# Optimization experiments

Hardware: AMD Instinct MI355X
Metric: run time of the kernel (lower is better)

## Reference

```python
import jax, jax.numpy as jnp
import numpy as np

B, N, DIM, HEADS = 8, 512, 512, 16
MAX_DIST, NG = 128, 32
RBF_STOP = 20.0
EPS = 1e-5


def _ln(x, g, b):
    m = jnp.mean(x, axis=-1, keepdims=True)
    v = jnp.mean((x - m) ** 2, axis=-1, keepdims=True)
    return (x - m) * jax.lax.rsqrt(v + EPS) * g + b


def setup_inputs() -> dict:
    key = jax.random.key(0)
    ks = jax.random.split(key, 12)
    d = DIM
    s = 0.02
    return {
        "x": jax.random.normal(ks[0], (B * N, d), jnp.float32),
        "dist_matrix": jax.random.randint(ks[1], (B, N, N), 0, MAX_DIST, jnp.int32),
        "dist_3d": jax.random.uniform(ks[2], (B, N, N), jnp.float32) * RBF_STOP,
        "norm1_g": jnp.ones((d,), jnp.float32),
        "norm1_b": jnp.zeros((d,), jnp.float32),
        "in_proj_w": jax.random.normal(ks[3], (3 * d, d), jnp.float32) * s,
        "in_proj_b": jnp.zeros((3 * d,), jnp.float32),
        "out_proj_w": jax.random.normal(ks[4], (d, d), jnp.float32) * s,
        "out_proj_b": jnp.zeros((d,), jnp.float32),
        "dist_emb": jax.random.normal(ks[5], (MAX_DIST, HEADS), jnp.float32) * s,
        "rbf_w": jax.random.normal(ks[6], (HEADS, NG), jnp.float32) * s,
        "rbf_b": jnp.zeros((HEADS,), jnp.float32),
        "norm2_g": jnp.ones((d,), jnp.float32),
        "norm2_b": jnp.zeros((d,), jnp.float32),
        "ffn_w1": jax.random.normal(ks[7], (4 * d, d), jnp.float32) * s,
        "ffn_b1": jnp.zeros((4 * d,), jnp.float32),
        "ffn_w2": jax.random.normal(ks[8], (d, 4 * d), jnp.float32) * s,
        "ffn_b2": jnp.zeros((d,), jnp.float32),
        "batch": jnp.repeat(jnp.arange(B, dtype=jnp.int32), N),
    }


def reference(x, dist_matrix, dist_3d, norm1_g, norm1_b, in_proj_w, in_proj_b,
              out_proj_w, out_proj_b, dist_emb, rbf_w, rbf_b, norm2_g, norm2_b,
              ffn_w1, ffn_b1, ffn_w2, ffn_b2, batch):
    b, n = dist_matrix.shape[0], dist_matrix.shape[1]
    d = x.shape[-1]
    dh = d // HEADS
    # equal-size graphs -> to_dense_batch is a reshape, mask all-true
    xd = x.reshape(b, n, d)

    # additive attention bias: shortest-path-distance embedding + RBF projection
    dc = jnp.clip(dist_matrix, 0, MAX_DIST - 1)
    bias_spd = dist_emb[dc]                                  # [b, n, n, H]
    offset = jnp.linspace(0.0, RBF_STOP, NG, dtype=jnp.float32)
    coeff = -0.5 / (RBF_STOP / (NG - 1)) ** 2
    rbf = jnp.exp(coeff * (dist_3d[..., None] - offset) ** 2)  # [b, n, n, NG]
    bias_3d = rbf @ rbf_w.T + rbf_b                          # [b, n, n, H]
    bias = jnp.transpose(bias_spd + bias_3d, (0, 3, 1, 2))   # [b, H, n, n]

    # multi-head attention (pre-norm residual, as in source)
    h = _ln(xd, norm1_g, norm1_b)
    qkv = h @ in_proj_w.T + in_proj_b
    q, k, v = jnp.split(qkv, 3, axis=-1)
    q = q.reshape(b, n, HEADS, dh).transpose(0, 2, 1, 3)
    k = k.reshape(b, n, HEADS, dh).transpose(0, 2, 1, 3)
    v = v.reshape(b, n, HEADS, dh).transpose(0, 2, 1, 3)
    scores = jnp.einsum('bhqd,bhkd->bhqk', q, k) / jnp.sqrt(jnp.float32(dh)) + bias
    attn = jax.nn.softmax(scores, axis=-1)
    ctx = jnp.einsum('bhqk,bhkd->bhqd', attn, v)
    ctx = ctx.transpose(0, 2, 1, 3).reshape(b, n, d)
    attn_out = ctx @ out_proj_w.T + out_proj_b
    h = h + attn_out

    # FFN (dropout inactive at eval)
    h2 = _ln(h, norm2_g, norm2_b)
    ff = jax.nn.gelu(h2 @ ffn_w1.T + ffn_b1, approximate=False) @ ffn_w2.T + ffn_b2
    h = h + ff
    return h.reshape(b * n, d)
```

## Files before the change

### kernel.cpp

```cpp
#include <hip/hip_runtime.h>
#include <hip/hip_bf16.h>
#include <math.h>

#define BB 8
#define NN 512
#define DD 512
#define NH 16
#define DH 32
#define TD 1536
#define NG 32
#define MAXD 128

typedef __attribute__((ext_vector_type(8))) short bf16x8;
typedef __attribute__((ext_vector_type(4))) float f32x4;
typedef __attribute__((ext_vector_type(2))) unsigned int u32x2;
typedef __attribute__((ext_vector_type(4))) unsigned int u32x4;

__device__ inline short f2bf(float x) {
    __hip_bfloat16 h = __float2bfloat16(x);
    return *reinterpret_cast<short*>(&h);
}
__device__ inline float bf2f(short x) {
    union { unsigned u; float f; } c;
    c.u = ((unsigned)(unsigned short)x) << 16;
    return c.f;
}
__device__ inline unsigned cvt_pk_bf16(float lo, float hi) {
    unsigned r;
    asm("v_cvt_pk_bf16_f32 %0, %1, %2" : "=v"(r) : "v"(lo), "v"(hi));
    return r;
}
__device__ inline float exp2fast(float x) {
    float r;
    asm("v_exp_f32 %0, %1" : "=v"(r) : "v"(x));
    return r;
}

__device__ inline void gld_lds16(const void* g, void* l) {
    __builtin_amdgcn_global_load_lds(
        (const __attribute__((address_space(1))) unsigned int*)g,
        (__attribute__((address_space(3))) unsigned int*)l, 16, 0, 0);
}

__global__ __launch_bounds__(256) void cvt_weights(
    const float* __restrict__ s0, const float* __restrict__ s1,
    const float* __restrict__ s2, const float* __restrict__ s3,
    short* __restrict__ d0, short* __restrict__ d1,
    short* __restrict__ d2, short* __restrict__ d3,
    const float* __restrict__ rbfw, const float* __restrict__ rbfb,
    short* __restrict__ Tg,
    int n0, int n1, int n2, int n3) {
    if (blockIdx.y == 4) {
        if (blockIdx.x != 0) return;
        const float STEP  = 20.0f / 31.0f;
        const float COEFF = -0.5f / (STEP * STEP);
        for (int idx = threadIdx.x; idx < 194 * 16; idx += 256) {
            const int i = idx >> 4, h = idx & 15;
            const float x = fminf((float)i, 192.0f) * (20.0f / 192.0f);
            float acc = rbfb[h];
#pragma unroll
            for (int g = 0; g < NG; g++) {
                const float t = x - (float)g * STEP;
                acc += __expf(COEFF * t * t) * rbfw[h * NG + g];
            }
            Tg[idx] = f2bf(acc * 1.44269504088896f);
        }
        return;
    }
    const float* s; short* d; int n;
    switch (blockIdx.y) {
        case 0: s = s0; d = d0; n = n0; break;
        case 1: s = s1; d = d1; n = n1; break;
        case 2: s = s2; d = d2; n = n2; break;
        default: s = s3; d = d3; n = n3; break;
    }
    const int i = (blockIdx.x * 256 + threadIdx.x) * 8;
    if (i >= n) return;
    const float4 a = *(const float4*)(s + i);
    const float4 b = *(const float4*)(s + i + 4);
    u32x4 o;
    o[0] = cvt_pk_bf16(a.x, a.y);
    o[1] = cvt_pk_bf16(a.z, a.w);
    o[2] = cvt_pk_bf16(b.x, b.y);
    o[3] = cvt_pk_bf16(b.z, b.w);
    *(u32x4*)(d + i) = o;
}

__global__ __launch_bounds__(256) void ln_kernel(const float* __restrict__ x,
                                                 const float* __restrict__ g,
                                                 const float* __restrict__ b,
                                                 short* __restrict__ out_bf) {
    const int row = blockIdx.x;
    const int tid = threadIdx.x;
    const int wave = tid >> 6, lane = tid & 63;
    const float* xr = x + (size_t)row * DD;
    const float2 v01 = *(const float2*)(xr + 2 * tid);
    float s = v01.x + v01.y, q = v01.x * v01.x + v01.y * v01.y;
#pragma unroll
    for (int m = 1; m < 64; m <<= 1) { s += __shfl_xor(s, m); q += __shfl_xor(q, m); }
    __shared__ float ps[8];
    if (lane == 0) { ps[wave] = s; ps[wave + 4] = q; }
    __syncthreads();
    s = ps[0] + ps[1] + ps[2] + ps[3];
    q = ps[4] + ps[5] + ps[6] + ps[7];
    const float mean = s * (1.0f / DD);
    const float var  = q * (1.0f / DD) - mean * mean;
    const float rs   = rsqrtf(var + 1e-5f);
    const float2 g2 = *(const float2*)(g + 2 * tid);
    const float2 b2 = *(const float2*)(b + 2 * tid);
    const float o0 = (v01.x - mean) * rs * g2.x + b2.x;
    const float o1 = (v01.y - mean) * rs * g2.y + b2.y;
    *(unsigned*)&out_bf[(size_t)row * DD + 2 * tid] = cvt_pk_bf16(o0, o1);
}

template <int TM, bool GELU, int RESMODE, bool OUTBF>
__global__ __launch_bounds__(256) void gemm_bf16(
    const short* __restrict__ A, const short* __restrict__ Bw,
    const float* __restrict__ bias, const void* __restrict__ res,
    void* __restrict__ Cout, int M, int Nout, int K) {
    const int MI = (TM >= 32) ? TM / 32 : 1;
    const int bm = blockIdx.y * TM;
    const int bn = blockIdx.x * 128;
    const int tid  = threadIdx.x;
    const int wave = tid >> 6;
    const int lane = tid & 63;
    const int l16  = lane & 15;
    const int quad = lane >> 4;
    const int wr = (wave >> 1) * (TM / 2);
    const int wc = (wave & 1) * 64;

    __shared__ short As[2][TM * 32];
    __shared__ short Bs[2][128 * 32];

    f32x4 acc[MI][4];
#pragma unroll
    for (int i = 0; i < MI; i++)
#pragma unroll
        for (int j = 0; j < 4; j++) acc[i][j] = (f32x4){0.f, 0.f, 0.f, 0.f};

    auto stage = [&](int buf, int k0) {
        const short* Ab = A + (size_t)bm * K + k0;
        const short* Bb = Bw + (size_t)bn * K + k0;
        if (TM >= 64) {
#pragma unroll
            for (int j = 0; j < TM / 64; j++) {
                const int idx = j * 256 + tid;
                gld_lds16(Ab + (size_t)(idx >> 2) * K + (idx & 3) * 8,
                          &As[buf][(size_t)(j * 256 + wave * 64) * 8]);
            }
        } else {
            if (tid < 128)
                gld_lds16(Ab + (size_t)(tid >> 2) * K + (tid & 3) * 8,
                          &As[buf][(size_t)(wave * 64) * 8]);
        }
#pragma unroll
        for (int j = 0; j < 2; j++) {
            const int idx = j * 256 + tid;
            gld_lds16(Bb + (size_t)(idx >> 2) * K + (idx & 3) * 8,
                      &Bs[buf][(size_t)(j * 256 + wave * 64) * 8]);
        }
    };
    auto compute = [&](int buf) {
        bf16x8 af[MI], bfr[4];
#pragma unroll
        for (int i = 0; i < MI; i++)
            af[i] = *(const bf16x8*)&As[buf][(wr + i * 16 + l16) * 32 + quad * 8];
#pragma unroll
        for (int j = 0; j < 4; j++)
            bfr[j] = *(const bf16x8*)&Bs[buf][(wc + j * 16 + l16) * 32 + quad * 8];
#pragma unroll
        for (int i = 0; i < MI; i++)
#pragma unroll
            for (int j = 0; j < 4; j++)
                acc[i][j] = __builtin_amdgcn_mfma_f32_16x16x32_bf16(bfr[j], af[i], acc[i][j], 0, 0, 0);
    };

    stage(0, 0);
    __syncthreads();
    int cur = 0;
    for (int k0 = 32; k0 < K; k0 += 32) {
        stage(cur ^ 1, k0);
        compute(cur);
        __syncthreads();
        cur ^= 1;
    }
    compute(cur);

#pragma unroll
    for (int i = 0; i < MI; i++) {
        const int row = bm + wr + i * 16 + l16;
#pragma unroll
        for (int j = 0; j < 4; j++) {
            const int col = bn + wc + j * 16 + quad * 4;
            const float4 b4 = *(const float4*)&bias[col];
            float v[4] = {acc[i][j][0] + b4.x, acc[i][j][1] + b4.y,
                          acc[i][j][2] + b4.z, acc[i][j][3] + b4.w};
            if (GELU) {
#pragma unroll
                for (int r = 0; r < 4; r++)
                    v[r] = 0.5f * v[r] * (1.0f + erff(v[r] * 0.70710678118654752f));
            }
            if (RESMODE == 1) {
                const float4 r4 = *(const float4*)&((const float*)res)[(size_t)row * Nout + col];
                v[0] += r4.x; v[1] += r4.y; v[2] += r4.z; v[3] += r4.w;
            }
            if (RESMODE == 2) {
                const short4 r4 = *(const short4*)&((const short*)res)[(size_t)row * Nout + col];
                v[0] += bf2f(r4.x); v[1] += bf2f(r4.y); v[2] += bf2f(r4.z); v[3] += bf2f(r4.w);
            }
            if (OUTBF) {
                u32x2 o;
                o[0] = cvt_pk_bf16(v[0], v[1]);
                o[1] = cvt_pk_bf16(v[2], v[3]);
                *(u32x2*)&((short*)Cout)[(size_t)row * Nout + col] = o;
            } else {
                *(float4*)&((float*)Cout)[(size_t)row * Nout + col] =
                    (float4){v[0], v[1], v[2], v[3]};
            }
        }
    }
}

__global__ __launch_bounds__(512, 2) void attn_mfma(
    const short* __restrict__ qkv,
    const int* __restrict__ dist,
    const float* __restrict__ dist3d,
    const float* __restrict__ demb,
    const short* __restrict__ Tg,
    short* __restrict__ Obf) {
    const int blk  = blockIdx.x;
    const int b    = blk & 7;
    const int q0   = (blk >> 3) * 16;
    const int tid  = threadIdx.x;
    const int wave = tid >> 6;
    const int lane = tid & 63;
    const int l16  = lane & 15;
    const int quad = lane >> 4;
    const int hh0  = wave * 2;

    __shared__ short Vc[2][NH * 1024];
    __shared__ short Pb[16 * 512];
    __shared__ short Tt[194 * 18];
    __shared__ short Db[128 * 18];
    __shared__ unsigned short Pk[512 * 16];

    for (int i = tid; i < 194 * 16; i += 512) Tt[(i >> 4) * 18 + (i & 15)] = Tg[i];
    for (int i = tid; i < 128 * 16; i += 512)
        Db[(i >> 4) * 18 + (i & 15)] = f2bf(demb[i] * 1.44269504088896f);
    {
        const size_t rb = ((size_t)(b * NN) + q0) * NN;
#pragma unroll
        for (int q = 0; q < 16; q++) {
            const size_t off = rb + (size_t)q * NN + tid;
            int dc = dist[off];
            dc = min(max(dc, 0), MAXD - 1);
            int ii = (int)(dist3d[off] * 9.6f + 0.5f);
            ii = min(ii, 192);
            Pk[tid * 16 + q] = (unsigned short)(dc | (ii << 8));
        }
    }

    const float scale = 0.17677669529663687f * 1.44269504088896f;
    bf16x8 qf[2];
#pragma unroll
    for (int h = 0; h < 2; h++)
        qf[h] = *(const bf16x8*)(qkv + (size_t)(b * NN + q0 + l16) * TD + (hh0 + h) * DH + quad * 8);

    f32x4 O[2][2];
    float lsum[2][4];
#pragma unroll
    for (int h = 0; h < 2; h++) {
#pragma unroll
        for (int tt = 0; tt < 2; tt++) O[h][tt] = (f32x4){0.f, 0.f, 0.f, 0.f};
#pragma unroll
        for (int r = 0; r < 4; r++) lsum[h][r] = 0.f;
    }

    __syncthreads();

    const int sk = lane >> 2;
    const int sc = lane & 3;

    auto stageV = [&](int buf, int c) {
        const size_t rowb = (size_t)(b * NN + c * 32 + sk) * TD + 2 * DD + sc * 8;
#pragma unroll
        for (int h = 0; h < 2; h++) {
            short* dst = &Vc[buf][(hh0 + h) * 1024];
            gld_lds16(qkv + rowb + (hh0 + h) * DH, dst);
            gld_lds16(qkv + rowb + (size_t)16 * TD + (hh0 + h) * DH, dst + 512);
        }
    };
    auto loadK = [&](int c, bf16x8 (*kd)[2]) {
#pragma unroll
        for (int h = 0; h < 2; h++) {
            const short* base =
                qkv + (size_t)(b * NN + c * 32 + l16) * TD + DD + (hh0 + h) * DH + quad * 8;
            kd[h][0] = *(const bf16x8*)base;
            kd[h][1] = *(const bf16x8*)(base + 16 * TD);
        }
    };

    bf16x8 kf[2][2], kfn[2][2];
    stageV(0, 0);
    loadK(0, kf);
    int cur = 0;

    for (int c = 0; c < 16; c++) {
        asm volatile("" ::: "memory");
        __builtin_amdgcn_s_waitcnt(0x0F70);
        asm volatile("" ::: "memory");

        u32x2 vraw[2][4];
#pragma unroll
        for (int h = 0; h < 2; h++) {
            const unsigned va =
                (unsigned)(uintptr_t)&Vc[cur][(hh0 + h) * 1024 + quad * 128 + l16];
            asm volatile("ds_read_b64_tr_b16 %0, %1 offset:0"    : "=v"(vraw[h][0]) : "v"(va));
            asm volatile("ds_read_b64_tr_b16 %0, %1 offset:128"  : "=v"(vraw[h][1]) : "v"(va));
            asm volatile("ds_read_b64_tr_b16 %0, %1 offset:1024" : "=v"(vraw[h][2]) : "v"(va));
            asm volatile("ds_read_b64_tr_b16 %0, %1 offset:1152" : "=v"(vraw[h][3]) : "v"(va));
        }

        if (c + 1 < 16) {
            stageV(cur ^ 1, c + 1);
            loadK(c + 1, kfn);
        }

#pragma unroll
        for (int half = 0; half < 2; half++) {
            const ushort4 pk4 =
                *(const ushort4*)&Pk[(unsigned)((c * 32 + half * 16 + l16) * 16 + quad * 4)];
            const unsigned short pe[4] = {pk4.x, pk4.y, pk4.z, pk4.w};
            float bb[2][4];
#pragma unroll
            for (int r = 0; r < 4; r++) {
                const unsigned u  = pe[r];
                const unsigned dc = u & 0xFFu;
                const unsigned ii = u >> 8;
                const unsigned du = *(const unsigned*)&Db[dc * 18 + hh0];
                const unsigned tu = *(const unsigned*)&Tt[ii * 18 + hh0];
                union { unsigned x; float f; } a0, a1, b0, b1;
                a0.x = du << 16; a1.x = du & 0xFFFF0000u;
                b0.x = tu << 16; b1.x = tu & 0xFFFF0000u;
                bb[0][r] = a0.f + b0.f;
                bb[1][r] = a1.f + b1.f;
            }
#pragma unroll
            for (int h = 0; h < 2; h++) {
                f32x4 s = __builtin_amdgcn_mfma_f32_16x16x32_bf16(
                    qf[h], kf[h][half], (f32x4){0.f, 0.f, 0.f, 0.f}, 0, 0, 0);
                float pv[4];
#pragma unroll
                for (int r = 0; r < 4; r++) {
                    float sv = s[r] * scale + bb[h][r];
                    sv = fminf(sv, 28.853901f);
                    pv[r] = exp2fast(sv);
                    lsum[h][r] += pv[r];
                }
                u32x2 w;
                w[0] = cvt_pk_bf16(pv[0], pv[1]);
                w[1] = cvt_pk_bf16(pv[2], pv[3]);
                *(u32x2*)&Pb[(wave * 2 + h) * 512 + (half * 16 + l16) * 16 + quad * 4] = w;
            }
        }

        asm volatile("" ::: "memory");
        asm volatile("s_waitcnt lgkmcnt(0)" ::: "memory");
        __builtin_amdgcn_sched_barrier(0);

        u32x2 praw[2][2];
#pragma unroll
        for (int h = 0; h < 2; h++) {
            const unsigned pa =
                (unsigned)(uintptr_t)&Pb[(wave * 2 + h) * 512 + quad * 64 + l16];
            asm volatile("ds_read_b64_tr_b16 %0, %1 offset:0"   : "=v"(praw[h][0]) : "v"(pa));
            asm volatile("ds_read_b64_tr_b16 %0, %1 offset:512" : "=v"(praw[h][1]) : "v"(pa));
        }
        asm volatile("s_waitcnt lgkmcnt(0)" ::: "memory");
        __builtin_amdgcn_sched_barrier(0);

        __builtin_amdgcn_s_setprio(1);
#pragma unroll
        for (int h = 0; h < 2; h++) {
            union { u32x4 u; bf16x8 s; } pf, v0, v1;
            pf.u = (u32x4){praw[h][0][0], praw[h][0][1], praw[h][1][0], praw[h][1][1]};
#pragma unroll
            for (int r = 0; r < 4; r++) {
                v0.u[r] = __builtin_amdgcn_perm(vraw[h][r][1], vraw[h][r][0], 0x05040100u);
                v1.u[r] = __builtin_amdgcn_perm(vraw[h][r][1], vraw[h][r][0], 0x07060302u);
            }
            O[h][0] = __builtin_amdgcn_mfma_f32_16x16x32_bf16(pf.s, v0.s, O[h][0], 0, 0, 0);
            O[h][1] = __builtin_amdgcn_mfma_f32_16x16x32_bf16(pf.s, v1.s, O[h][1], 0, 0, 0);
        }
        __builtin_amdgcn_s_setprio(0);

#pragma unroll
        for (int h = 0; h < 2; h++) { kf[h][0] = kfn[h][0]; kf[h][1] = kfn[h][1]; }
        cur ^= 1;
    }

#pragma unroll
    for (int h = 0; h < 2; h++) {
        const int hh = hh0 + h;
#pragma unroll
        for (int m = 1; m < 16; m <<= 1)
#pragma unroll
            for (int r = 0; r < 4; r++) lsum[h][r] += __shfl_xor(lsum[h][r], m);
#pragma unroll
        for (int r = 0; r < 4; r++) {
            const float rl = 1.0f / lsum[h][r];
            const size_t row = (size_t)(b * NN + q0 + quad * 4 + r);
#pragma unroll
            for (int tt = 0; tt < 2; tt++)
                Obf[row * DD + hh * DH + tt * 16 + l16] = f2bf(O[h][tt][r] * rl);
        }
    }
}

extern "C" void kernel_launch(void* const* d_in, const int* in_sizes, int n_in,
                              void* d_out, int out_size, void* d_ws, size_t ws_size,
                              hipStream_t stream) {
    const float* x      = (const float*)d_in[0];
    const int*   dist   = (const int*)d_in[1];
    const float* dist3d = (const float*)d_in[2];
    const float* n1g    = (const float*)d_in[3];
    const float* n1b    = (const float*)d_in[4];
    const float* win    = (const float*)d_in[5];
    const float* bin    = (const float*)d_in[6];
    const float* wo     = (const float*)d_in[7];
    const float* bo     = (const float*)d_in[8];
    const float* demb   = (const float*)d_in[9];
    const float* rbfw   = (const float*)d_in[10];
    const float* rbfb   = (const float*)d_in[11];
    const float* n2g    = (const float*)d_in[12];
    const float* n2b    = (const float*)d_in[13];
    const float* w1     = (const float*)d_in[14];
    const float* b1     = (const float*)d_in[15];
    const float* w2     = (const float*)d_in[16];
    const float* b2     = (const float*)d_in[17];

    char* p = (char*)d_ws;
    short* h_bf   = (short*)p; p += (size_t)4096 * 512 * 2;
    short* qkv_bf = (short*)p; p += (size_t)4096 * 1536 * 2;
    float* hres   = (float*)p; p += (size_t)4096 * 512 * 4;
    short* h2_bf  = (short*)p; p += (size_t)4096 * 512 * 2;
    short* win_bf = (short*)p; p += (size_t)1536 * 512 * 2;
    short* wo_bf  = (short*)p; p += (size_t)512 * 512 * 2;
    short* w1_bf  = (short*)p; p += (size_t)2048 * 512 * 2;
    short* w2_bf  = (short*)p; p += (size_t)512 * 2048 * 2;
    short* Tg     = (short*)p; p += (size_t)8192;
    short* o_bf   = (short*)p;
    short* mid_bf = (short*)p;
    p += (size_t)4096 * 2048 * 2;

    const int M = BB * NN;

    cvt_weights<<<dim3(512, 5), 256, 0, stream>>>(
        win, wo, w1, w2, win_bf, wo_bf, w1_bf, w2_bf, rbfw, rbfb, Tg,
        1536 * 512, 512 * 512, 2048 * 512, 512 * 2048);
    ln_kernel<<<M, 256, 0, stream>>>(x, n1g, n1b, h_bf);
    gemm_bf16<64, false, 0, true><<<dim3(12, 64), 256, 0, stream>>>(
        h_bf, win_bf, bin, nullptr, qkv_bf, M, TD, DD);
    attn_mfma<<<256, 512, 0, stream>>>(
        qkv_bf, dist, dist3d, demb, Tg, o_bf);
    gemm_bf16<32, false, 2, false><<<dim3(4, 128), 256, 0, stream>>>(
        o_bf, wo_bf, bo, h_bf, hres, M, DD, DD);
    ln_kernel<<<M, 256, 0, stream>>>(hres, n2g, n2b, h2_bf);
    gemm_bf16<128, true, 0, true><<<dim3(16, 32), 256, 0, stream>>>(
        h2_bf, w1_bf, b1, nullptr, mid_bf, M, 2048, DD);
    gemm_bf16<32, false, 1, false><<<dim3(4, 128), 256, 0, stream>>>(
        mid_bf, w2_bf, b2, hres, (float*)d_out, M, DD, 2048);
}
```

Baseline: 241.6 us.

## Split-K the FFN down-projection with larger tiles and a separate combine kernel

```diff
diff --git a/kernel.cpp b/kernel.cpp
--- a/kernel.cpp
+++ b/kernel.cpp
@@ -113,14 +113,15 @@
     *(unsigned*)&out_bf[(size_t)row * DD + 2 * tid] = cvt_pk_bf16(o0, o1);
 }
 
-template <int TM, bool GELU, int RESMODE, bool OUTBF>
+template <int TM, bool GELU, int RESMODE, bool OUTBF, bool PARTIAL>
 __global__ __launch_bounds__(256) void gemm_bf16(
     const short* __restrict__ A, const short* __restrict__ Bw,
     const float* __restrict__ bias, const void* __restrict__ res,
-    void* __restrict__ Cout, int M, int Nout, int K) {
+    void* __restrict__ Cout, int M, int Nout, int K, int Kloop) {
     const int MI = (TM >= 32) ? TM / 32 : 1;
     const int bm = blockIdx.y * TM;
     const int bn = blockIdx.x * 128;
+    const int kbase = PARTIAL ? blockIdx.z * Kloop : 0;
     const int tid  = threadIdx.x;
     const int wave = tid >> 6;
     const int lane = tid & 63;
@@ -139,8 +140,8 @@
         for (int j = 0; j < 4; j++) acc[i][j] = (f32x4){0.f, 0.f, 0.f, 0.f};
 
     auto stage = [&](int buf, int k0) {
-        const short* Ab = A + (size_t)bm * K + k0;
-        const short* Bb = Bw + (size_t)bn * K + k0;
+        const short* Ab = A + (size_t)bm * K + kbase + k0;
+        const short* Bb = Bw + (size_t)bn * K + kbase + k0;
         if (TM >= 64) {
 #pragma unroll
             for (int j = 0; j < TM / 64; j++) {
@@ -178,7 +179,7 @@
     stage(0, 0);
     __syncthreads();
     int cur = 0;
-    for (int k0 = 32; k0 < K; k0 += 32) {
+    for (int k0 = 32; k0 < Kloop; k0 += 32) {
         stage(cur ^ 1, k0);
         compute(cur);
         __syncthreads();
@@ -186,15 +187,20 @@
     }
     compute(cur);
 
+    float* pout = PARTIAL
+        ? (float*)Cout + (size_t)blockIdx.z * M * Nout
+        : (float*)Cout;
 #pragma unroll
     for (int i = 0; i < MI; i++) {
         const int row = bm + wr + i * 16 + l16;
 #pragma unroll
         for (int j = 0; j < 4; j++) {
             const int col = bn + wc + j * 16 + quad * 4;
-            const float4 b4 = *(const float4*)&bias[col];
-            float v[4] = {acc[i][j][0] + b4.x, acc[i][j][1] + b4.y,
-                          acc[i][j][2] + b4.z, acc[i][j][3] + b4.w};
+            float v[4] = {acc[i][j][0], acc[i][j][1], acc[i][j][2], acc[i][j][3]};
+            if (!PARTIAL) {
+                const float4 b4 = *(const float4*)&bias[col];
+                v[0] += b4.x; v[1] += b4.y; v[2] += b4.z; v[3] += b4.w;
+            }
             if (GELU) {
 #pragma unroll
                 for (int r = 0; r < 4; r++)
@@ -214,11 +220,29 @@
                 o[1] = cvt_pk_bf16(v[2], v[3]);
                 *(u32x2*)&((short*)Cout)[(size_t)row * Nout + col] = o;
             } else {
-                *(float4*)&((float*)Cout)[(size_t)row * Nout + col] =
-                    (float4){v[0], v[1], v[2], v[3]};
-            }
-        }
-    }
+                *(float4*)&pout[(size_t)row * Nout + col] = (float4){v[0], v[1], v[2], v[3]};
+            }
+        }
+    }
+}
+
+__global__ __launch_bounds__(256) void combine4(
+    const float* __restrict__ p, const float* __restrict__ bias,
+    const float* __restrict__ res, float* __restrict__ out) {
+    const size_t PO = (size_t)4096 * 512;
+    const size_t i = ((size_t)blockIdx.x * 256 + threadIdx.x) * 4;
+    const float4 a = *(const float4*)(p + i);
+    const float4 b = *(const float4*)(p + PO + i);
+    const float4 c = *(const float4*)(p + 2 * PO + i);
+    const float4 d = *(const float4*)(p + 3 * PO + i);
+    const float4 r = *(const float4*)(res + i);
+    const float4 bb = *(const float4*)&bias[i & 511];
+    float4 o;
+    o.x = a.x + b.x + c.x + d.x + r.x + bb.x;
+    o.y = a.y + b.y + c.y + d.y + r.y + bb.y;
+    o.z = a.z + b.z + c.z + d.z + r.z + bb.z;
+    o.w = a.w + b.w + c.w + d.w + r.w + bb.w;
+    *(float4*)(out + i) = o;
 }
 
 __global__ __launch_bounds__(512, 2) void attn_mfma(
@@ -452,6 +476,7 @@
     short* o_bf   = (short*)p;
     short* mid_bf = (short*)p;
     p += (size_t)4096 * 2048 * 2;
+    float* fpart  = (float*)p; p += (size_t)4 * 4096 * 512 * 4;
 
     const int M = BB * NN;
 
@@ -459,15 +484,16 @@
         win, wo, w1, w2, win_bf, wo_bf, w1_bf, w2_bf, rbfw, rbfb, Tg,
         1536 * 512, 512 * 512, 2048 * 512, 512 * 2048);
     ln_kernel<<<M, 256, 0, stream>>>(x, n1g, n1b, h_bf);
-    gemm_bf16<64, false, 0, true><<<dim3(12, 64), 256, 0, stream>>>(
-        h_bf, win_bf, bin, nullptr, qkv_bf, M, TD, DD);
+    gemm_bf16<128, false, 0, true, false><<<dim3(12, 32), 256, 0, stream>>>(
+        h_bf, win_bf, bin, nullptr, qkv_bf, M, TD, DD, DD);
     attn_mfma<<<256, 512, 0, stream>>>(
         qkv_bf, dist, dist3d, demb, Tg, o_bf);
-    gemm_bf16<32, false, 2, false><<<dim3(4, 128), 256, 0, stream>>>(
-        o_bf, wo_bf, bo, h_bf, hres, M, DD, DD);
+    gemm_bf16<32, false, 2, false, false><<<dim3(4, 128), 256, 0, stream>>>(
+        o_bf, wo_bf, bo, h_bf, hres, M, DD, DD, DD);
     ln_kernel<<<M, 256, 0, stream>>>(hres, n2g, n2b, h2_bf);
-    gemm_bf16<128, true, 0, true><<<dim3(16, 32), 256, 0, stream>>>(
-        h2_bf, w1_bf, b1, nullptr, mid_bf, M, 2048, DD);
-    gemm_bf16<32, false, 1, false><<<dim3(4, 128), 256, 0, stream>>>(
-        mid_bf, w2_bf, b2, hres, (float*)d_out, M, DD, 2048);
-}
+    gemm_bf16<128, true, 0, true, false><<<dim3(16, 32), 256, 0, stream>>>(
+        h2_bf, w1_bf, b1, nullptr, mid_bf, M, 2048, DD, DD);
+    gemm_bf16<128, false, 0, false, true><<<dim3(4, 32, 4), 256, 0, stream>>>(
+        mid_bf, w2_bf, nullptr, nullptr, fpart, M, DD, 2048, DD);
+    combine4<<<2048, 256, 0, stream>>>(fpart, b2, hres, (float*)d_out);
+}
```

Result: no change. 237.8 us (-1.6%).

## Fuse out-projection and second LayerNorm into attention; merge LN1 with weight prep

Applied to the files above, without the earlier changes.

```diff
diff --git a/kernel.cpp b/kernel.cpp
--- a/kernel.cpp
+++ b/kernel.cpp
@@ -42,7 +42,9 @@
         (__attribute__((address_space(3))) unsigned int*)l, 16, 0, 0);
 }
 
-__global__ __launch_bounds__(256) void cvt_weights(
+__global__ __launch_bounds__(256) void prep(
+    const float* __restrict__ x, const float* __restrict__ n1g,
+    const float* __restrict__ n1b, short* __restrict__ h_bf,
     const float* __restrict__ s0, const float* __restrict__ s1,
     const float* __restrict__ s2, const float* __restrict__ s3,
     short* __restrict__ d0, short* __restrict__ d1,
@@ -50,17 +52,43 @@
     const float* __restrict__ rbfw, const float* __restrict__ rbfb,
     short* __restrict__ Tg,
     int n0, int n1, int n2, int n3) {
-    if (blockIdx.y == 4) {
-        if (blockIdx.x != 0) return;
+    const int tid = threadIdx.x;
+    if (blockIdx.x < 4096) {
+        const int row = blockIdx.x;
+        const int wave = tid >> 6, lane = tid & 63;
+        const float* xr = x + (size_t)row * DD;
+        const float2 v01 = *(const float2*)(xr + 2 * tid);
+        float s = v01.x + v01.y, q = v01.x * v01.x + v01.y * v01.y;
+#pragma unroll
+        for (int m = 1; m < 64; m <<= 1) { s += __shfl_xor(s, m); q += __shfl_xor(q, m); }
+        __shared__ float ps[8];
+        if (lane == 0) { ps[wave] = s; ps[wave + 4] = q; }
+        __syncthreads();
+        s = ps[0] + ps[1] + ps[2] + ps[3];
+        q = ps[4] + ps[5] + ps[6] + ps[7];
+        const float mean = s * (1.0f / DD);
+        const float var  = q * (1.0f / DD) - mean * mean;
+        const float rs   = rsqrtf(var + 1e-5f);
+        const float2 g2 = *(const float2*)(n1g + 2 * tid);
+        const float2 b2 = *(const float2*)(n1b + 2 * tid);
+        const float o0 = (v01.x - mean) * rs * g2.x + b2.x;
+        const float o1 = (v01.y - mean) * rs * g2.y + b2.y;
+        *(unsigned*)&h_bf[(size_t)row * DD + 2 * tid] = cvt_pk_bf16(o0, o1);
+        return;
+    }
+    const int bx = blockIdx.x - 4096;
+    const int y = bx >> 9, xb = bx & 511;
+    if (y == 4) {
+        if (xb != 0) return;
         const float STEP  = 20.0f / 31.0f;
         const float COEFF = -0.5f / (STEP * STEP);
-        for (int idx = threadIdx.x; idx < 194 * 16; idx += 256) {
+        for (int idx = tid; idx < 194 * 16; idx += 256) {
             const int i = idx >> 4, h = idx & 15;
-            const float x = fminf((float)i, 192.0f) * (20.0f / 192.0f);
+            const float xx = fminf((float)i, 192.0f) * (20.0f / 192.0f);
             float acc = rbfb[h];
 #pragma unroll
             for (int g = 0; g < NG; g++) {
-                const float t = x - (float)g * STEP;
+                const float t = xx - (float)g * STEP;
                 acc += __expf(COEFF * t * t) * rbfw[h * NG + g];
             }
             Tg[idx] = f2bf(acc * 1.44269504088896f);
@@ -68,13 +96,13 @@
         return;
     }
     const float* s; short* d; int n;
-    switch (blockIdx.y) {
+    switch (y) {
         case 0: s = s0; d = d0; n = n0; break;
         case 1: s = s1; d = d1; n = n1; break;
         case 2: s = s2; d = d2; n = n2; break;
         default: s = s3; d = d3; n = n3; break;
     }
-    const int i = (blockIdx.x * 256 + threadIdx.x) * 8;
+    const int i = (xb * 256 + tid) * 8;
     if (i >= n) return;
     const float4 a = *(const float4*)(s + i);
     const float4 b = *(const float4*)(s + i + 4);
@@ -84,33 +112,6 @@
     o[2] = cvt_pk_bf16(b.x, b.y);
     o[3] = cvt_pk_bf16(b.z, b.w);
     *(u32x4*)(d + i) = o;
-}
-
-__global__ __launch_bounds__(256) void ln_kernel(const float* __restrict__ x,
-                                                 const float* __restrict__ g,
-                                                 const float* __restrict__ b,
-                                                 short* __restrict__ out_bf) {
-    const int row = blockIdx.x;
-    const int tid = threadIdx.x;
-    const int wave = tid >> 6, lane = tid & 63;
-    const float* xr = x + (size_t)row * DD;
-    const float2 v01 = *(const float2*)(xr + 2 * tid);
-    float s = v01.x + v01.y, q = v01.x * v01.x + v01.y * v01.y;
-#pragma unroll
-    for (int m = 1; m < 64; m <<= 1) { s += __shfl_xor(s, m); q += __shfl_xor(q, m); }
-    __shared__ float ps[8];
-    if (lane == 0) { ps[wave] = s; ps[wave + 4] = q; }
-    __syncthreads();
-    s = ps[0] + ps[1] + ps[2] + ps[3];
-    q = ps[4] + ps[5] + ps[6] + ps[7];
-    const float mean = s * (1.0f / DD);
-    const float var  = q * (1.0f / DD) - mean * mean;
-    const float rs   = rsqrtf(var + 1e-5f);
-    const float2 g2 = *(const float2*)(g + 2 * tid);
-    const float2 b2 = *(const float2*)(b + 2 * tid);
-    const float o0 = (v01.x - mean) * rs * g2.x + b2.x;
-    const float o1 = (v01.y - mean) * rs * g2.y + b2.y;
-    *(unsigned*)&out_bf[(size_t)row * DD + 2 * tid] = cvt_pk_bf16(o0, o1);
 }
 
 template <int TM, bool GELU, int RESMODE, bool OUTBF>
@@ -221,13 +222,19 @@
     }
 }
 
-__global__ __launch_bounds__(512, 2) void attn_mfma(
+__global__ __launch_bounds__(512, 2) void attn_fused(
     const short* __restrict__ qkv,
     const int* __restrict__ dist,
     const float* __restrict__ dist3d,
     const float* __restrict__ demb,
     const short* __restrict__ Tg,
-    short* __restrict__ Obf) {
+    const short* __restrict__ wo,
+    const float* __restrict__ bo,
+    const short* __restrict__ hb,
+    const float* __restrict__ g2v,
+    const float* __restrict__ b2v,
+    float* __restrict__ hres,
+    short* __restrict__ h2) {
     const int blk  = blockIdx.x;
     const int b    = blk & 7;
     const int q0   = (blk >> 3) * 16;
@@ -243,6 +250,7 @@
     __shared__ short Tt[194 * 18];
     __shared__ short Db[128 * 18];
     __shared__ unsigned short Pk[512 * 16];
+    __shared__ float St[2][16][8];
 
     for (int i = tid; i < 194 * 16; i += 512) Tt[(i >> 4) * 18 + (i & 15)] = Tg[i];
     for (int i = tid; i < 128 * 16; i += 512)
@@ -401,18 +409,101 @@
 
 #pragma unroll
     for (int h = 0; h < 2; h++) {
-        const int hh = hh0 + h;
 #pragma unroll
         for (int m = 1; m < 16; m <<= 1)
 #pragma unroll
             for (int r = 0; r < 4; r++) lsum[h][r] += __shfl_xor(lsum[h][r], m);
+        float rl[4];
+#pragma unroll
+        for (int r = 0; r < 4; r++) rl[r] = 1.0f / lsum[h][r];
+#pragma unroll
+        for (int tt = 0; tt < 2; tt++) {
+            const int col = (hh0 + h) * DH + tt * 16 + l16;
+            u32x2 w;
+            w[0] = cvt_pk_bf16(O[h][tt][0] * rl[0], O[h][tt][1] * rl[1]);
+            w[1] = cvt_pk_bf16(O[h][tt][2] * rl[2], O[h][tt][3] * rl[3]);
+            *(u32x2*)&Pb[col * 16 + quad * 4] = w;
+        }
+    }
+    __syncthreads();
+
+    f32x4 a2[4];
+#pragma unroll
+    for (int j = 0; j < 4; j++) a2[j] = (f32x4){0.f, 0.f, 0.f, 0.f};
+    const int wcol = wave * 64;
+    for (int k0 = 0; k0 < DD; k0 += 32) {
+        u32x2 p0, p1;
+        const unsigned pa = (unsigned)(uintptr_t)&Pb[k0 * 16 + quad * 64 + l16];
+        asm volatile("ds_read_b64_tr_b16 %0, %1 offset:0"   : "=v"(p0) : "v"(pa));
+        asm volatile("ds_read_b64_tr_b16 %0, %1 offset:512" : "=v"(p1) : "v"(pa));
+        u32x2 blo[4], bhi[4];
+#pragma unroll
+        for (int j = 0; j < 4; j++) {
+            const short* wb = wo + (size_t)(wcol + j * 16 + l16) * DD + k0 + quad * 4;
+            blo[j] = *(const u32x2*)wb;
+            bhi[j] = *(const u32x2*)(wb + 16);
+        }
+        asm volatile("s_waitcnt lgkmcnt(0)" ::: "memory");
+        __builtin_amdgcn_sched_barrier(0);
+        union { u32x4 u; bf16x8 s; } af;
+        af.u = (u32x4){p0[0], p0[1], p1[0], p1[1]};
+#pragma unroll
+        for (int j = 0; j < 4; j++) {
+            union { u32x4 u; bf16x8 s; } bw;
+            bw.u = (u32x4){blo[j][0], blo[j][1], bhi[j][0], bhi[j][1]};
+            a2[j] = __builtin_amdgcn_mfma_f32_16x16x32_bf16(af.s, bw.s, a2[j], 0, 0, 0);
+        }
+    }
+
+    const int rowg = b * NN + q0;
+    float vv[4][4];
+    float sp[4] = {0.f, 0.f, 0.f, 0.f}, qp[4] = {0.f, 0.f, 0.f, 0.f};
+#pragma unroll
+    for (int j = 0; j < 4; j++) {
+        const int col = wcol + j * 16 + l16;
+        const float bc = bo[col];
 #pragma unroll
         for (int r = 0; r < 4; r++) {
-            const float rl = 1.0f / lsum[h][r];
-            const size_t row = (size_t)(b * NN + q0 + quad * 4 + r);
-#pragma unroll
-            for (int tt = 0; tt < 2; tt++)
-                Obf[row * DD + hh * DH + tt * 16 + l16] = f2bf(O[h][tt][r] * rl);
+            const size_t row = (size_t)rowg + quad * 4 + r;
+            const float v = a2[j][r] + bc + bf2f(hb[row * DD + col]);
+            hres[row * DD + col] = v;
+            vv[j][r] = v;
+            sp[r] += v; qp[r] += v * v;
+        }
+    }
+#pragma unroll
+    for (int m = 1; m < 16; m <<= 1)
+#pragma unroll
+        for (int r = 0; r < 4; r++) {
+            sp[r] += __shfl_xor(sp[r], m);
+            qp[r] += __shfl_xor(qp[r], m);
+        }
+    if (l16 == 0) {
+#pragma unroll
+        for (int r = 0; r < 4; r++) {
+            St[0][quad * 4 + r][wave] = sp[r];
+            St[1][quad * 4 + r][wave] = qp[r];
+        }
+    }
+    __syncthreads();
+    float mean[4], rsd[4];
+#pragma unroll
+    for (int r = 0; r < 4; r++) {
+        const int rr = quad * 4 + r;
+        float s = 0.f, q = 0.f;
+#pragma unroll
+        for (int w = 0; w < 8; w++) { s += St[0][rr][w]; q += St[1][rr][w]; }
+        mean[r] = s * (1.0f / DD);
+        rsd[r]  = rsqrtf(q * (1.0f / DD) - mean[r] * mean[r] + 1e-5f);
+    }
+#pragma unroll
+    for (int j = 0; j < 4; j++) {
+        const int col = wcol + j * 16 + l16;
+        const float gc = g2v[col], bc2 = b2v[col];
+#pragma unroll
+        for (int r = 0; r < 4; r++) {
+            const size_t row = (size_t)rowg + quad * 4 + r;
+            h2[row * DD + col] = f2bf((vv[j][r] - mean[r]) * rsd[r] * gc + bc2);
         }
     }
 }
@@ -449,23 +540,18 @@
     short* w1_bf  = (short*)p; p += (size_t)2048 * 512 * 2;
     short* w2_bf  = (short*)p; p += (size_t)512 * 2048 * 2;
     short* Tg     = (short*)p; p += (size_t)8192;
-    short* o_bf   = (short*)p;
-    short* mid_bf = (short*)p;
-    p += (size_t)4096 * 2048 * 2;
+    short* mid_bf = (short*)p; p += (size_t)4096 * 2048 * 2;
 
     const int M = BB * NN;
 
-    cvt_weights<<<dim3(512, 5), 256, 0, stream>>>(
+    prep<<<4096 + 2560, 256, 0, stream>>>(
+        x, n1g, n1b, h_bf,
         win, wo, w1, w2, win_bf, wo_bf, w1_bf, w2_bf, rbfw, rbfb, Tg,
         1536 * 512, 512 * 512, 2048 * 512, 512 * 2048);
-    ln_kernel<<<M, 256, 0, stream>>>(x, n1g, n1b, h_bf);
-    gemm_bf16<64, false, 0, true><<<dim3(12, 64), 256, 0, stream>>>(
+    gemm_bf16<128, false, 0, true><<<dim3(12, 32), 256, 0, stream>>>(
         h_bf, win_bf, bin, nullptr, qkv_bf, M, TD, DD);
-    attn_mfma<<<256, 512, 0, stream>>>(
-        qkv_bf, dist, dist3d, demb, Tg, o_bf);
-    gemm_bf16<32, false, 2, false><<<dim3(4, 128), 256, 0, stream>>>(
-        o_bf, wo_bf, bo, h_bf, hres, M, DD, DD);
-    ln_kernel<<<M, 256, 0, stream>>>(hres, n2g, n2b, h2_bf);
+    attn_fused<<<256, 512, 0, stream>>>(
+        qkv_bf, dist, dist3d, demb, Tg, wo_bf, bo, h_bf, n2g, n2b, hres, h2_bf);
     gemm_bf16<128, true, 0, true><<<dim3(16, 32), 256, 0, stream>>>(
         h2_bf, w1_bf, b1, nullptr, mid_bf, M, 2048, DD);
     gemm_bf16<32, false, 1, false><<<dim3(4, 128), 256, 0, stream>>>(
```

New measurement: 258.6 us. 7.0% more time.
